# Kernel optimization log

Hardware: AMD Instinct MI355X
Metric: run time of the kernel (lower is better)

The kernel has to match this reference:

```python
import jax, jax.numpy as jnp
import numpy as np

B, T, N_EMBD, N_HEAD = 2, 2048, 1024, 16
HEAD = N_EMBD // N_HEAD
WINDOW = 64


def setup_inputs() -> dict:
    key = jax.random.key(0)
    kq, kk, kv, kw = jax.random.split(key, 4)
    q = jax.random.normal(kq, (B, T, N_EMBD), dtype=jnp.float32)
    k = jax.random.normal(kk, (B, T, N_EMBD), dtype=jnp.float32)
    v = jax.random.normal(kv, (B, T, N_EMBD), dtype=jnp.float32)
    W_proj = jax.random.normal(kw, (N_EMBD, N_EMBD), dtype=jnp.float32) * (1.0 / np.sqrt(N_EMBD))
    b_proj = jnp.zeros((N_EMBD,), dtype=jnp.float32)
    return {"q": q, "k": k, "v": v, "W_proj": W_proj, "b_proj": b_proj}


def reference(q, k, v, W_proj, b_proj):
    Bsz, Tlen, _ = q.shape
    # split heads: [B, H, T, D]
    qh = q.reshape(Bsz, Tlen, N_HEAD, HEAD).transpose(0, 2, 1, 3)
    kh = k.reshape(Bsz, Tlen, N_HEAD, HEAD).transpose(0, 2, 1, 3)
    vh = v.reshape(Bsz, Tlen, N_HEAD, HEAD).transpose(0, 2, 1, 3)

    scale = 1.0 / np.sqrt(HEAD)
    scores = jnp.einsum('bhqd,bhkd->bhqk', qh, kh) * scale  # [B,H,T,T]

    # windowed additive mask: positions with |i-j| > WINDOW get -inf
    idx = jnp.arange(Tlen)
    dist = jnp.abs(idx[None, :] - idx[:, None])  # [T, T]
    scores = jnp.where(dist[None, None] > WINDOW, -jnp.inf, scores)

    attn = jax.nn.softmax(scores, axis=-1)
    y = jnp.einsum('bhqk,bhkd->bhqd', attn, vh)  # [B,H,T,D]
    y = y.transpose(0, 2, 1, 3).reshape(Bsz, Tlen, N_EMBD)
    return y @ W_proj.T + b_proj
```

## Files before the change

### kernel.cpp

```cpp
#include <hip/hip_runtime.h>
#include <hip/hip_bf16.h>

#define B_SZ 2
#define T_SZ 2048
#define NE   1024
#define NH   16
#define HD   64
#define WIN  64
#define QT   64
#define KT   192
#define GM   4096
#define GN   1024
#define GK   1024
#define KPAD 72
#define VPAD 200

__device__ ushort Wb_static[GN * GK];

__device__ __forceinline__ uint pack2(float lo, float hi) {
    uint r;
    asm("v_cvt_pk_bf16_f32 %0, %1, %2" : "=v"(r) : "v"(lo), "v"(hi));
    return r;
}
__device__ __forceinline__ uint4 pack8(float4 a, float4 b) {
    return make_uint4(pack2(a.x, a.y), pack2(a.z, a.w),
                      pack2(b.x, b.y), pack2(b.z, b.w));
}

typedef __attribute__((ext_vector_type(8))) short frag_ab;
typedef __attribute__((ext_vector_type(4))) float frag_cd;
union FragU { frag_ab f; uint u[4]; };

#define LDS_BAR() do {                                        \
    asm volatile("s_waitcnt lgkmcnt(0)" ::: "memory");        \
    __builtin_amdgcn_s_barrier();                             \
    asm volatile("" ::: "memory");                            \
} while (0)

__global__ __launch_bounds__(256, 3) void attn_mfma_kernel(
    const float* __restrict__ q, const float* __restrict__ k,
    const float* __restrict__ v, const float* __restrict__ W,
    ushort* __restrict__ y)
{
    __shared__ __attribute__((aligned(16))) ushort pool[KT * KPAD + HD * VPAD];
    ushort* Ks = pool;
    ushort* Vt = pool + KT * KPAD;
    ushort* Ps = pool;

    const int bid = blockIdx.x;
    const int swz = ((bid & 7) << 7) | (bid >> 3);
    const int qs  = (swz & 31) * QT;
    const int h   = (swz >> 5) & 15;
    const int b   = swz >> 9;
    const int t   = threadIdx.x;
    const int kstart = qs - WIN;

    const int wv   = t >> 6;
    const int L    = t & 63;
    const int r16  = L & 15;
    const int quad = L >> 4;

    float4 qf0, qf1, qg0, qg1;
    {
        const float* qrow = q + ((size_t)(b * T_SZ + qs + wv * 16 + r16)) * NE + h * HD;
        const float4* p0 = (const float4*)(qrow + quad * 8);
        const float4* p1 = (const float4*)(qrow + 32 + quad * 8);
        qf0 = p0[0]; qf1 = p0[1]; qg0 = p1[0]; qg1 = p1[1];
    }

    {
        const int idx = bid * 256 + t;
        const float4 f = ((const float4*)W)[idx];
        ((uint2*)Wb_static)[idx] = make_uint2(pack2(f.x, f.y), pack2(f.z, f.w));
    }

    float4 va[6], vb[6];
#pragma unroll
    for (int i = 0; i < 6; ++i) {
        const int c  = t + 256 * i;
        const int j  = c >> 3;
        const int cc = c & 7;
        const int d8 = cc * 8;
        const int jg = kstart + j;
        const int jc = min(max(jg, 0), T_SZ - 1);
        const size_t off = ((size_t)(b * T_SZ + jc)) * NE + h * HD + d8;
        const float4* kp = (const float4*)(k + off);
        const float4* vp = (const float4*)(v + off);
        va[i] = vp[0]; vb[i] = vp[1];
        const float4 k0 = kp[0], k1 = kp[1];
        *(uint4*)&Ks[j * KPAD + d8] = pack8(k0, k1);
    }

    const float QSC = 0.125f * 1.44269504f;
    frag_ab aq0, aq1;
    {
        FragU u0, u1;
        u0.u[0] = pack2(qf0.x * QSC, qf0.y * QSC);
        u0.u[1] = pack2(qf0.z * QSC, qf0.w * QSC);
        u0.u[2] = pack2(qf1.x * QSC, qf1.y * QSC);
        u0.u[3] = pack2(qf1.z * QSC, qf1.w * QSC);
        u1.u[0] = pack2(qg0.x * QSC, qg0.y * QSC);
        u1.u[1] = pack2(qg0.z * QSC, qg0.w * QSC);
        u1.u[2] = pack2(qg1.x * QSC, qg1.y * QSC);
        u1.u[3] = pack2(qg1.z * QSC, qg1.w * QSC);
        aq0 = u0.f; aq1 = u1.f;
    }
    LDS_BAR();

    frag_cd sacc[12];
#pragma unroll
    for (int nb = 0; nb < 12; ++nb) sacc[nb] = (frag_cd){0,0,0,0};
    __builtin_amdgcn_s_setprio(1);
#pragma unroll
    for (int nb = 0; nb < 12; ++nb) {
        const frag_ab b0 = *(const frag_ab*)&Ks[(nb * 16 + r16) * KPAD + quad * 8];
        const frag_ab b1 = *(const frag_ab*)&Ks[(nb * 16 + r16) * KPAD + 32 + quad * 8];
        sacc[nb] = __builtin_amdgcn_mfma_f32_16x16x32_bf16(aq0, b0, sacc[nb], 0, 0, 0);
        sacc[nb] = __builtin_amdgcn_mfma_f32_16x16x32_bf16(aq1, b1, sacc[nb], 0, 0, 0);
    }
    __builtin_amdgcn_s_setprio(0);

    const int base_m = wv * 16 + quad * 4;
    float l[4] = {0.f, 0.f, 0.f, 0.f};
#pragma unroll
    for (int nb = 0; nb < 12; ++nb) {
        const int jl = nb * 16 + r16;
        const int jg = kstart + jl;
        const bool jg_ok = (jg >= 0) & (jg < T_SZ);
#pragma unroll
        for (int r = 0; r < 4; ++r) {
            const int mrow = base_m + r;
            const bool valid = jg_ok & ((uint)(jl - mrow) <= 2u * WIN);
            const float p = valid ? exp2f(sacc[nb][r]) : 0.0f;
            l[r] += p;
            sacc[nb][r] = p;
        }
    }
#pragma unroll
    for (int r = 0; r < 4; ++r) {
        l[r] += __shfl_xor(l[r], 1);
        l[r] += __shfl_xor(l[r], 2);
        l[r] += __shfl_xor(l[r], 4);
        l[r] += __shfl_xor(l[r], 8);
    }

#pragma unroll
    for (int i = 0; i < 6; ++i) {
        const int c  = t + 256 * i;
        const int j  = c >> 3;
        const int cc = c & 7;
        const int d8 = cc * 8;
        ushort* vtc = &Vt[d8 * VPAD + (((j >> 3) ^ cc) * 8 + (j & 7))];
        const uint p01 = pack2(va[i].x, va[i].y);
        const uint p23 = pack2(va[i].z, va[i].w);
        const uint p45 = pack2(vb[i].x, vb[i].y);
        const uint p67 = pack2(vb[i].z, vb[i].w);
        vtc[0 * VPAD] = (ushort)p01; vtc[1 * VPAD] = (ushort)(p01 >> 16);
        vtc[2 * VPAD] = (ushort)p23; vtc[3 * VPAD] = (ushort)(p23 >> 16);
        vtc[4 * VPAD] = (ushort)p45; vtc[5 * VPAD] = (ushort)(p45 >> 16);
        vtc[6 * VPAD] = (ushort)p67; vtc[7 * VPAD] = (ushort)(p67 >> 16);
    }

    LDS_BAR();
#pragma unroll
    for (int nb = 0; nb < 12; ++nb) {
        const int jl = nb * 16 + r16;
        const uint p01 = pack2(sacc[nb][0], sacc[nb][1]);
        const uint p23 = pack2(sacc[nb][2], sacc[nb][3]);
        Ps[(base_m + 0) * VPAD + jl] = (ushort)p01;
        Ps[(base_m + 1) * VPAD + jl] = (ushort)(p01 >> 16);
        Ps[(base_m + 2) * VPAD + jl] = (ushort)p23;
        Ps[(base_m + 3) * VPAD + jl] = (ushort)(p23 >> 16);
    }
    LDS_BAR();

    frag_ab ap[6];
#pragma unroll
    for (int kb = 0; kb < 6; ++kb)
        ap[kb] = *(const frag_ab*)&Ps[(wv * 16 + r16) * VPAD + kb * 32 + quad * 8];

    frag_cd oacc[4];
#pragma unroll
    for (int nb = 0; nb < 4; ++nb) oacc[nb] = (frag_cd){0,0,0,0};
    __builtin_amdgcn_s_setprio(1);
#pragma unroll
    for (int nb = 0; nb < 4; ++nb) {
        const int dr  = nb * 16 + r16;
        const int dsw = (dr >> 3) & 7;
#pragma unroll
        for (int kb = 0; kb < 6; ++kb) {
            const frag_ab bv = *(const frag_ab*)&Vt[dr * VPAD + (((kb * 4 + quad) ^ dsw) * 8)];
            oacc[nb] = __builtin_amdgcn_mfma_f32_16x16x32_bf16(ap[kb], bv, oacc[nb], 0, 0, 0);
        }
    }
    __builtin_amdgcn_s_setprio(0);

    float inv[4];
#pragma unroll
    for (int r = 0; r < 4; ++r) inv[r] = 1.0f / l[r];
#pragma unroll
    for (int nb = 0; nb < 4; ++nb) {
        const int d  = nb * 16 + r16;
        const uint p01 = pack2(oacc[nb][0] * inv[0], oacc[nb][1] * inv[1]);
        const uint p23 = pack2(oacc[nb][2] * inv[2], oacc[nb][3] * inv[3]);
        const size_t rb = (size_t)(b * T_SZ + qs + base_m) * NE + h * HD + d;
        y[rb + 0 * NE] = (ushort)p01;
        y[rb + 1 * NE] = (ushort)(p01 >> 16);
        y[rb + 2 * NE] = (ushort)p23;
        y[rb + 3 * NE] = (ushort)(p23 >> 16);
    }
}

#define ASZ (128 * 64)
#define BSZ (64 * 64)

__global__ __launch_bounds__(256, 2) void proj_gemm_kernel(
    const ushort* __restrict__ A,
    const float* __restrict__ bias, float* __restrict__ C)
{
    __shared__ __attribute__((aligned(16))) ushort As[2 * ASZ];
    __shared__ __attribute__((aligned(16))) ushort Bs[2 * BSZ];

    const ushort* Bw = Wb_static;
    const int t   = threadIdx.x;
    const int bid = blockIdx.x;
    const int swz = ((bid & 7) << 6) | (bid >> 3);
    const int tile_n = swz & 15;
    const int tile_m = swz >> 4;
    const int lane   = t & 63;
    const int wv     = t >> 6;
    const int wm     = wv >> 1;
    const int wn     = wv & 1;
    const int r16    = lane & 15;
    const int quad   = lane >> 4;

    frag_cd acc[4][2];
#pragma unroll
    for (int mi = 0; mi < 4; ++mi)
#pragma unroll
        for (int ni = 0; ni < 2; ++ni)
            acc[mi][ni] = (frag_cd){0.0f, 0.0f, 0.0f, 0.0f};

    const int fm = wm * 64 + r16;
    const int fn = wn * 32 + r16;
    const int sw = r16 & 7;

#define STAGE_AB(buf, kk)                                                      \
    {                                                                          \
        _Pragma("unroll")                                                      \
        for (int i = 0; i < 4; ++i) {                                          \
            const int c   = t + 256 * i;                                       \
            const int row = c >> 3;                                            \
            const int src = ((c & 7) ^ (row & 7)) * 8;                         \
            __builtin_amdgcn_global_load_lds(                                  \
                (const __attribute__((address_space(1))) unsigned int*)        \
                    (A + (size_t)(tile_m * 128 + row) * GK + (kk) + src),      \
                (__attribute__((address_space(3))) unsigned int*)              \
                    (As + (buf) * ASZ + c * 8), 16, 0, 0);                     \
        }                                                                      \
        _Pragma("unroll")                                                      \
        for (int i = 0; i < 2; ++i) {                                          \
            const int c   = t + 256 * i;                                       \
            const int row = c >> 3;                                            \
            const int src = ((c & 7) ^ (row & 7)) * 8;                         \
            __builtin_amdgcn_global_load_lds(                                  \
                (const __attribute__((address_space(1))) unsigned int*)        \
                    (Bw + (size_t)(tile_n * 64 + row) * GK + (kk) + src),      \
                (__attribute__((address_space(3))) unsigned int*)              \
                    (Bs + (buf) * BSZ + c * 8), 16, 0, 0);                     \
        }                                                                      \
    }

#define COMPUTE_AB(buf)                                                        \
    {                                                                          \
        _Pragma("unroll")                                                      \
        for (int ks = 0; ks < 2; ++ks) {                                       \
            const int cidx = (((ks * 4) + quad) ^ sw) * 8;                     \
            frag_ab af[4], bfr[2];                                             \
            _Pragma("unroll")                                                  \
            for (int mi = 0; mi < 4; ++mi)                                     \
                af[mi] = *(const frag_ab*)                                     \
                    &As[(buf) * ASZ + (fm + mi * 16) * 64 + cidx];             \
            _Pragma("unroll")                                                  \
            for (int ni = 0; ni < 2; ++ni)                                     \
                bfr[ni] = *(const frag_ab*)                                    \
                    &Bs[(buf) * BSZ + (fn + ni * 16) * 64 + cidx];             \
            _Pragma("unroll")                                                  \
            for (int mi = 0; mi < 4; ++mi)                                     \
                _Pragma("unroll")                                              \
                for (int ni = 0; ni < 2; ++ni)                                 \
                    acc[mi][ni] = __builtin_amdgcn_mfma_f32_16x16x32_bf16(     \
                        af[mi], bfr[ni], acc[mi][ni], 0, 0, 0);                \
        }                                                                      \
    }

    STAGE_AB(0, 0);
    __syncthreads();

    for (int k0 = 0; k0 < GK; k0 += 128) {
        STAGE_AB(1, k0 + 64);
        COMPUTE_AB(0);
        __syncthreads();
        if (k0 + 128 < GK) STAGE_AB(0, k0 + 128);
        COMPUTE_AB(1);
        __syncthreads();
    }

#pragma unroll
    for (int mi = 0; mi < 4; ++mi) {
#pragma unroll
        for (int ni = 0; ni < 2; ++ni) {
            const int rbase = tile_m * 128 + wm * 64 + mi * 16 + quad * 4;
            const int cg    = tile_n * 64 + wn * 32 + ni * 16 + r16;
            const float bv  = bias[cg];
#pragma unroll
            for (int r = 0; r < 4; ++r)
                C[(size_t)(rbase + r) * GN + cg] = acc[mi][ni][r] + bv;
        }
    }
}

extern "C" void kernel_launch(void* const* d_in, const int* in_sizes, int n_in,
                              void* d_out, int out_size, void* d_ws, size_t ws_size,
                              hipStream_t stream) {
    (void)in_sizes; (void)n_in; (void)out_size; (void)ws_size;
    const float* q    = (const float*)d_in[0];
    const float* k    = (const float*)d_in[1];
    const float* v    = (const float*)d_in[2];
    const float* W    = (const float*)d_in[3];
    const float* bias = (const float*)d_in[4];
    float*  out = (float*)d_out;
    ushort* y   = (ushort*)d_ws;

    dim3 g1(1024);
    attn_mfma_kernel<<<g1, 256, 0, stream>>>(q, k, v, W, y);

    dim3 g2(512);
    proj_gemm_kernel<<<g2, 256, 0, stream>>>(y, bias, out);
}
```

Baseline: 120.7 us.

## Restrict attention MFMAs to in-window key blocks and relax GEMM pipeline barriers

Result: no change. 119.1 us, median of 2 (-1.3%).

```diff
diff --git a/kernel.cpp b/kernel.cpp
--- a/kernel.cpp
+++ b/kernel.cpp
@@ -37,6 +37,12 @@
     asm volatile("" ::: "memory");                            \
 } while (0)
 
+#define VM_BAR(N) do {                                        \
+    asm volatile("s_waitcnt vmcnt(" #N ")" ::: "memory");     \
+    __builtin_amdgcn_s_barrier();                             \
+    asm volatile("" ::: "memory");                            \
+} while (0)
+
 __global__ __launch_bounds__(256, 3) void attn_mfma_kernel(
     const float* __restrict__ q, const float* __restrict__ k,
     const float* __restrict__ v, const float* __restrict__ W,
@@ -107,33 +113,34 @@
     }
     LDS_BAR();
 
-    frag_cd sacc[12];
-#pragma unroll
-    for (int nb = 0; nb < 12; ++nb) sacc[nb] = (frag_cd){0,0,0,0};
+    frag_cd sacc[9];
+#pragma unroll
+    for (int i = 0; i < 9; ++i) sacc[i] = (frag_cd){0,0,0,0};
     __builtin_amdgcn_s_setprio(1);
 #pragma unroll
-    for (int nb = 0; nb < 12; ++nb) {
+    for (int i = 0; i < 9; ++i) {
+        const int nb = wv + i;
         const frag_ab b0 = *(const frag_ab*)&Ks[(nb * 16 + r16) * KPAD + quad * 8];
         const frag_ab b1 = *(const frag_ab*)&Ks[(nb * 16 + r16) * KPAD + 32 + quad * 8];
-        sacc[nb] = __builtin_amdgcn_mfma_f32_16x16x32_bf16(aq0, b0, sacc[nb], 0, 0, 0);
-        sacc[nb] = __builtin_amdgcn_mfma_f32_16x16x32_bf16(aq1, b1, sacc[nb], 0, 0, 0);
+        sacc[i] = __builtin_amdgcn_mfma_f32_16x16x32_bf16(aq0, b0, sacc[i], 0, 0, 0);
+        sacc[i] = __builtin_amdgcn_mfma_f32_16x16x32_bf16(aq1, b1, sacc[i], 0, 0, 0);
     }
     __builtin_amdgcn_s_setprio(0);
 
     const int base_m = wv * 16 + quad * 4;
     float l[4] = {0.f, 0.f, 0.f, 0.f};
 #pragma unroll
-    for (int nb = 0; nb < 12; ++nb) {
-        const int jl = nb * 16 + r16;
+    for (int i = 0; i < 9; ++i) {
+        const int jl = (wv + i) * 16 + r16;
         const int jg = kstart + jl;
         const bool jg_ok = (jg >= 0) & (jg < T_SZ);
 #pragma unroll
         for (int r = 0; r < 4; ++r) {
             const int mrow = base_m + r;
             const bool valid = jg_ok & ((uint)(jl - mrow) <= 2u * WIN);
-            const float p = valid ? exp2f(sacc[nb][r]) : 0.0f;
+            const float p = valid ? exp2f(sacc[i][r]) : 0.0f;
             l[r] += p;
-            sacc[nb][r] = p;
+            sacc[i][r] = p;
         }
     }
 #pragma unroll
@@ -163,21 +170,29 @@
 
     LDS_BAR();
 #pragma unroll
-    for (int nb = 0; nb < 12; ++nb) {
-        const int jl = nb * 16 + r16;
-        const uint p01 = pack2(sacc[nb][0], sacc[nb][1]);
-        const uint p23 = pack2(sacc[nb][2], sacc[nb][3]);
+    for (int i = 0; i < 9; ++i) {
+        const int jl = (wv + i) * 16 + r16;
+        const uint p01 = pack2(sacc[i][0], sacc[i][1]);
+        const uint p23 = pack2(sacc[i][2], sacc[i][3]);
         Ps[(base_m + 0) * VPAD + jl] = (ushort)p01;
         Ps[(base_m + 1) * VPAD + jl] = (ushort)(p01 >> 16);
         Ps[(base_m + 2) * VPAD + jl] = (ushort)p23;
         Ps[(base_m + 3) * VPAD + jl] = (ushort)(p23 >> 16);
     }
+    {
+        const int zb = (wv & 1) ? (wv - 1) : (wv + 9);
+        const int jl = zb * 16 + r16;
+#pragma unroll
+        for (int r = 0; r < 4; ++r)
+            Ps[(base_m + r) * VPAD + jl] = 0;
+    }
     LDS_BAR();
 
-    frag_ab ap[6];
-#pragma unroll
-    for (int kb = 0; kb < 6; ++kb)
-        ap[kb] = *(const frag_ab*)&Ps[(wv * 16 + r16) * VPAD + kb * 32 + quad * 8];
+    const int kb0 = wv >> 1;
+    frag_ab ap[5];
+#pragma unroll
+    for (int i = 0; i < 5; ++i)
+        ap[i] = *(const frag_ab*)&Ps[(wv * 16 + r16) * VPAD + (kb0 + i) * 32 + quad * 8];
 
     frag_cd oacc[4];
 #pragma unroll
@@ -188,9 +203,10 @@
         const int dr  = nb * 16 + r16;
         const int dsw = (dr >> 3) & 7;
 #pragma unroll
-        for (int kb = 0; kb < 6; ++kb) {
+        for (int i = 0; i < 5; ++i) {
+            const int kb = kb0 + i;
             const frag_ab bv = *(const frag_ab*)&Vt[dr * VPAD + (((kb * 4 + quad) ^ dsw) * 8)];
-            oacc[nb] = __builtin_amdgcn_mfma_f32_16x16x32_bf16(ap[kb], bv, oacc[nb], 0, 0, 0);
+            oacc[nb] = __builtin_amdgcn_mfma_f32_16x16x32_bf16(ap[i], bv, oacc[nb], 0, 0, 0);
         }
     }
     __builtin_amdgcn_s_setprio(0);
@@ -295,15 +311,19 @@
     }
 
     STAGE_AB(0, 0);
-    __syncthreads();
-
-    for (int k0 = 0; k0 < GK; k0 += 128) {
-        STAGE_AB(1, k0 + 64);
-        COMPUTE_AB(0);
-        __syncthreads();
-        if (k0 + 128 < GK) STAGE_AB(0, k0 + 128);
-        COMPUTE_AB(1);
-        __syncthreads();
+    int cur = 0;
+    for (int k0 = 0; k0 < GK - 64; k0 += 64) {
+        STAGE_AB(cur ^ 1, k0 + 64);
+        VM_BAR(6);
+        COMPUTE_AB(cur);
+        LDS_BAR();
+        cur ^= 1;
+    }
+    {
+        asm volatile("s_waitcnt vmcnt(0)" ::: "memory");
+        __builtin_amdgcn_s_barrier();
+        asm volatile("" ::: "memory");
+        COMPUTE_AB(cur);
     }
 
 #pragma unroll
```
